# Performance work log

Hardware: AMD Instinct MI355X
Metric: run time of the kernel (lower is better)

Reference implementation:

```python
import jax, jax.numpy as jnp
import numpy as np

DIM = 1024
NUM_HEADS = 16
HEAD_D = DIM // NUM_HEADS


def setup_inputs() -> dict:
    key = jax.random.key(0)
    ks = jax.random.split(key, 9)
    s = 1.0 / np.sqrt(DIM)
    x = jax.random.normal(ks[0], (2, 2048, DIM), dtype=jnp.float32)
    Wq = jax.random.uniform(ks[1], (DIM, DIM), jnp.float32, -s, s)
    bq = jax.random.uniform(ks[2], (DIM,), jnp.float32, -s, s)
    Wk = jax.random.uniform(ks[3], (DIM, DIM), jnp.float32, -s, s)
    bk = jax.random.uniform(ks[4], (DIM,), jnp.float32, -s, s)
    Wv = jax.random.uniform(ks[5], (DIM, DIM), jnp.float32, -s, s)
    bv = jax.random.uniform(ks[6], (DIM,), jnp.float32, -s, s)
    Wo = jax.random.uniform(ks[7], (DIM, DIM), jnp.float32, -s, s)
    bo = jax.random.uniform(ks[8], (DIM,), jnp.float32, -s, s)
    return {"x": x, "Wq": Wq, "bq": bq, "Wk": Wk, "bk": bk,
            "Wv": Wv, "bv": bv, "Wo": Wo, "bo": bo}


def reference(x, Wq, bq, Wk, bk, Wv, bv, Wo, bo):
    B, T, D = x.shape
    H, Hd = NUM_HEADS, HEAD_D
    # torch Linear: x @ W.T + b
    q = (x @ Wq.T + bq).reshape(B, T, H, Hd).transpose(0, 2, 1, 3)  # [B,H,T,Hd]
    k = (x @ Wk.T + bk).reshape(B, T, H, Hd).transpose(0, 2, 1, 3)
    v = (x @ Wv.T + bv).reshape(B, T, H, Hd).transpose(0, 2, 1, 3)
    scores = jnp.einsum('bhqd,bhkd->bhqk', q, k) / jnp.sqrt(jnp.float32(Hd))
    causal = jnp.tril(jnp.ones((T, T), dtype=bool))  # [T,T]
    scores = jnp.where(causal[None, None], scores, -jnp.inf)
    probs = jax.nn.softmax(scores, axis=-1)
    ctx = jnp.einsum('bhqk,bhkd->bhqd', probs, v)
    out = ctx.transpose(0, 2, 1, 3).reshape(B, T, D)
    out = out @ Wo.T + bo
    return (out, (k, v))
```

## Files before the change

### kernel.cpp

```cpp
#include <hip/hip_runtime.h>

#define BB 2
#define TT 2048
#define DD 1024
#define HH 16
#define HD 64
#define MM (BB*TT)

typedef __bf16 bf16;
typedef __bf16 bf16x4 __attribute__((ext_vector_type(4)));
typedef __bf16 bf16x8 __attribute__((ext_vector_type(8)));
typedef float  f32x4  __attribute__((ext_vector_type(4)));

#define QSCALE 0.1803368801111244f
#define M0 16.0f

__device__ __forceinline__ void gl_lds16(const void* g, void* l) {
  __builtin_amdgcn_global_load_lds(
      (const __attribute__((address_space(1))) void*)g,
      (__attribute__((address_space(3))) void*)l, 16, 0, 0);
}
__device__ __forceinline__ f32x4 mfma16(bf16x8 a, bf16x8 b, f32x4 c) {
  return __builtin_amdgcn_mfma_f32_16x16x32_bf16(a, b, c, 0, 0, 0);
}

__global__ void cvt_all(const float* __restrict__ x,
                        const float* __restrict__ w0, const float* __restrict__ w1,
                        const float* __restrict__ w2, const float* __restrict__ w3,
                        bf16* __restrict__ xd,
                        bf16* __restrict__ d0, bf16* __restrict__ d1,
                        bf16* __restrict__ d2, bf16* __restrict__ d3) {
  int i = blockIdx.x * blockDim.x + threadIdx.x;
  const float* s;
  bf16* d;
  int off;
  if (i < (1 << 20)) { s = x; d = xd; off = i; }
  else {
    int j = (i - (1 << 20)) >> 18;
    off = (i - (1 << 20)) & ((1 << 18) - 1);
    s = (j == 0) ? w0 : (j == 1) ? w1 : (j == 2) ? w2 : w3;
    d = (j == 0) ? d0 : (j == 1) ? d1 : (j == 2) ? d2 : d3;
  }
  float4 v = ((const float4*)s)[off];
  bf16x4 o = { (bf16)v.x, (bf16)v.y, (bf16)v.z, (bf16)v.w };
  ((bf16x4*)d)[off] = o;
}

__launch_bounds__(512)
__global__ void gemm_qkv(const bf16* __restrict__ X,
                         const bf16* __restrict__ Wq, const bf16* __restrict__ Wk,
                         const bf16* __restrict__ Wv,
                         const float* __restrict__ bq, const float* __restrict__ bk,
                         const float* __restrict__ bv,
                         bf16* __restrict__ qb, bf16* __restrict__ kb,
                         bf16* __restrict__ vtb,
                         float* __restrict__ kf, float* __restrict__ vf) {
  __shared__ bf16 sA[128 * 32];
  __shared__ bf16 sB[2][128 * 32];
  const int tid  = threadIdx.x;
  const int wv   = tid >> 6;
  const int lane = tid & 63;
  const int quad = lane >> 4, l15 = lane & 15;
  const int wy   = wv >> 1, wx = wv & 1;
  const int g    = blockIdx.x >> 4;
  const int j    = blockIdx.x & 15;
  const int row  = tid >> 2;
  const int c8   = ((tid & 3) ^ ((row >> 1) & 3)) * 8;
  const int rsw  = (l15 >> 1) & 3;
  char* lA  = (char*)sA    + wv * 1024;
  char* lB0 = (char*)sB[0] + wv * 1024;
  char* lB1 = (char*)sB[1] + wv * 1024;

  if (j < 8) {
    const int m0 = g * 128;
    const int n0 = j * 128;
    const bf16* Ab  = X  + (size_t)(m0 + row) * DD + c8;
    const bf16* Bqb = Wq + (size_t)(n0 + row) * DD + c8;
    const bf16* Bkb = Wk + (size_t)(n0 + row) * DD + c8;
    f32x4 accq[2][4] = {}, acck[2][4] = {};
    for (int k0 = 0; k0 < DD; k0 += 32) {
      gl_lds16(Ab  + k0, lA);
      gl_lds16(Bqb + k0, lB0);
      gl_lds16(Bkb + k0, lB1);
      __syncthreads();
      bf16x8 af[2], bq_[4], bk_[4];
#pragma unroll
      for (int mi = 0; mi < 2; mi++)
        af[mi] = *(const bf16x8*)(sA + (wy * 32 + mi * 16 + l15) * 32
                                     + ((quad ^ rsw) * 8));
#pragma unroll
      for (int ni = 0; ni < 4; ni++) {
        bq_[ni] = *(const bf16x8*)(sB[0] + (wx * 64 + ni * 16 + l15) * 32
                                         + ((quad ^ rsw) * 8));
        bk_[ni] = *(const bf16x8*)(sB[1] + (wx * 64 + ni * 16 + l15) * 32
                                         + ((quad ^ rsw) * 8));
      }
#pragma unroll
      for (int mi = 0; mi < 2; mi++)
#pragma unroll
        for (int ni = 0; ni < 4; ni++) {
          accq[mi][ni] = mfma16(af[mi], bq_[ni], accq[mi][ni]);
          acck[mi][ni] = mfma16(af[mi], bk_[ni], acck[mi][ni]);
        }
      __syncthreads();
    }
    for (int mi = 0; mi < 2; mi++)
      for (int ni = 0; ni < 4; ni++)
        for (int r = 0; r < 4; r++) {
          int m = m0 + wy * 32 + mi * 16 + quad * 4 + r;
          int n = n0 + wx * 64 + ni * 16 + l15;
          int b = m >> 11, t = m & (TT - 1);
          int h = n >> 6,  d = n & (HD - 1);
          size_t idx = ((size_t)(b * HH + h) * TT + t) * HD + d;
          qb[idx] = (bf16)((accq[mi][ni][r] + bq[n]) * QSCALE);
          float vk = acck[mi][ni][r] + bk[n];
          kb[idx] = (bf16)vk;
          kf[idx] = vk;
        }
  } else {
    const int m0 = (j - 8) * 128;
    const int n0 = g * 128;
    const bf16* Ab = Wv + (size_t)(m0 + row) * DD + c8;
    const bf16* Bb = X  + (size_t)(n0 + row) * DD + c8;
    f32x4 acc[2][4] = {};
    for (int k0 = 0; k0 < DD; k0 += 32) {
      gl_lds16(Ab + k0, lA);
      gl_lds16(Bb + k0, lB0);
      __syncthreads();
      bf16x8 af[2], bx_[4];
#pragma unroll
      for (int mi = 0; mi < 2; mi++)
        af[mi] = *(const bf16x8*)(sA + (wy * 32 + mi * 16 + l15) * 32
                                     + ((quad ^ rsw) * 8));
#pragma unroll
      for (int ni = 0; ni < 4; ni++)
        bx_[ni] = *(const bf16x8*)(sB[0] + (wx * 64 + ni * 16 + l15) * 32
                                        + ((quad ^ rsw) * 8));
#pragma unroll
      for (int mi = 0; mi < 2; mi++)
#pragma unroll
        for (int ni = 0; ni < 4; ni++)
          acc[mi][ni] = mfma16(af[mi], bx_[ni], acc[mi][ni]);
      __syncthreads();
    }
    for (int mi = 0; mi < 2; mi++) {
      int mbase = m0 + wy * 32 + mi * 16 + quad * 4;
      float brv[4];
      for (int r = 0; r < 4; r++) brv[r] = bv[mbase + r];
      int h = mbase >> 6, dbase = mbase & (HD - 1);
      for (int ni = 0; ni < 4; ni++) {
        int tok = n0 + wx * 64 + ni * 16 + l15;
        int b = tok >> 11, t = tok & (TT - 1);
        int bh = b * HH + h;
        float4 vv;
        float* vp = &vv.x;
        for (int r = 0; r < 4; r++) {
          float v = acc[mi][ni][r] + brv[r];
          vp[r] = v;
          vtb[((size_t)bh * HD + dbase + r) * TT + t] = (bf16)v;
        }
        *(float4*)&vf[((size_t)bh * TT + t) * HD + dbase] = vv;
      }
    }
  }
}

template<int BM, int BN>
__device__ __forceinline__ void tile_core64(const bf16* __restrict__ A,
                                            const bf16* __restrict__ W,
                                            int m0, int n0,
                                            bf16* sA, bf16* sB,
                                            f32x4 (&acc)[BM/32][BN/32]) {
  const int tid  = threadIdx.x;
  const int wv   = tid >> 6;
  const int l15  = tid & 15;
  const int quad = (tid & 63) >> 4;
  const int wy   = wv >> 1, wx = wv & 1;
  const int MI_  = BM / 32, NI_ = BN / 32;
  const int srow = tid >> 3;
  const int schk = (tid & 7) ^ (srow & 7);
  const int rswz = l15 & 7;
  const bf16* Ab = A + (size_t)(m0 + srow) * DD + schk * 8;
  const bf16* Wb = W + (size_t)(n0 + srow) * DD + schk * 8;
  char* lA = (char*)sA + wv * 1024;
  char* lB = (char*)sB + wv * 1024;
  for (int k0 = 0; k0 < DD; k0 += 64) {
#pragma unroll
    for (int j = 0; j < BM / 32; j++)
      gl_lds16(Ab + (size_t)j * 32 * DD + k0, lA + j * 4096);
#pragma unroll
    for (int j = 0; j < BN / 32; j++)
      gl_lds16(Wb + (size_t)j * 32 * DD + k0, lB + j * 4096);
    __syncthreads();
#pragma unroll
    for (int h = 0; h < 2; h++) {
      bf16x8 af[MI_], bw[NI_];
#pragma unroll
      for (int mi = 0; mi < MI_; mi++)
        af[mi] = *(const bf16x8*)(sA + (wy * (BM / 2) + mi * 16 + l15) * 64
                                     + (((h * 4 + quad) ^ rswz) * 8));
#pragma unroll
      for (int ni = 0; ni < NI_; ni++)
        bw[ni] = *(const bf16x8*)(sB + (wx * (BN / 2) + ni * 16 + l15) * 64
                                     + (((h * 4 + quad) ^ rswz) * 8));
#pragma unroll
      for (int mi = 0; mi < MI_; mi++)
#pragma unroll
        for (int ni = 0; ni < NI_; ni++)
          acc[mi][ni] = mfma16(af[mi], bw[ni], acc[mi][ni]);
    }
    __syncthreads();
  }
}

__launch_bounds__(256)
__global__ void gemm_o(const bf16* __restrict__ A, const bf16* __restrict__ W,
                       const float* __restrict__ bias, float* __restrict__ out) {
  __shared__ bf16 sA[64 * 64];
  __shared__ bf16 sB[128 * 64];
  const int m0 = blockIdx.x * 64;
  const int n0 = blockIdx.y * 128;
  f32x4 acc[2][4] = {};
  tile_core64<64, 128>(A, W, m0, n0, sA, sB, acc);
  const int wv = threadIdx.x >> 6;
  const int l15 = threadIdx.x & 15, quad = (threadIdx.x & 63) >> 4;
  const int wy = wv >> 1, wx = wv & 1;
  for (int mi = 0; mi < 2; mi++)
    for (int ni = 0; ni < 4; ni++)
      for (int r = 0; r < 4; r++) {
        int m = m0 + wy * 32 + mi * 16 + quad * 4 + r;
        int n = n0 + wx * 64 + ni * 16 + l15;
        out[(size_t)m * DD + n] = acc[mi][ni][r] + bias[n];
      }
}

__launch_bounds__(256, 4)
__global__ void attn_fwd(const bf16* __restrict__ Q, const bf16* __restrict__ Kg,
                         const bf16* __restrict__ Vt, bf16* __restrict__ ctx) {
  __shared__ __align__(16) bf16 kbuf[2][4096];
  __shared__ __align__(16) bf16 vbuf[2][4096];
  __shared__ __align__(16) bf16 pbuf[4][1024];
  const int tid  = threadIdx.x;
  const int lane = tid & 63, wv = tid >> 6;
  const int quad = lane >> 4, l15 = lane & 15;
  const int bx = blockIdx.x;
  const int sl = bx >> 3;
  const int c  = 31 - (sl >> 2);
  const int bh = (bx & 7) + 8 * (sl & 3);
  const int qr = c * 64 + wv * 16;
  const int ntiles = c + 1;

  const bf16* Kbh = Kg + (size_t)bh * TT * HD;
  const bf16* Vbh = Vt + (size_t)bh * HD * TT;

  const int k0s = tid >> 3,  c0s = (tid & 7) ^ (k0s & 7);
  const int s1  = 256 + tid;
  const int k1s = s1 >> 3,   c1s = (s1 & 7) ^ (k1s & 7);

  int foff[4][2];
  for (int sub = 0; sub < 4; sub++)
    for (int h = 0; h < 2; h++)
      foff[sub][h] = (((sub * 16 + l15) * 8) + ((h * 4 + quad) ^ (l15 & 7))) * 8;

  const bf16* qp = Q + ((size_t)bh * TT + qr + l15) * HD + quad * 8;
  bf16x8 aq0 = *(const bf16x8*)qp;
  bf16x8 aq1 = *(const bf16x8*)(qp + 32);

  float lrow = 0.f;
  f32x4 acc[4] = {};
  bf16* pb = pbuf[wv];
  const int pswz = l15 & 7;

  gl_lds16(Kbh + (size_t)k0s * HD + c0s * 8, (char*)kbuf[0] + wv * 1024);
  gl_lds16(Kbh + (size_t)k1s * HD + c1s * 8, (char*)kbuf[0] + 4096 + wv * 1024);
  gl_lds16(Vbh + (size_t)k0s * TT + c0s * 8, (char*)vbuf[0] + wv * 1024);
  gl_lds16(Vbh + (size_t)k1s * TT + c1s * 8, (char*)vbuf[0] + 4096 + wv * 1024);

  for (int t = 0; t < ntiles; t++) {
    const int kt = t * 64;
    __syncthreads();
    if (t + 1 < ntiles) {
      bf16* kn = kbuf[(t + 1) & 1];
      bf16* vn = vbuf[(t + 1) & 1];
      gl_lds16(Kbh + (size_t)(kt + 64 + k0s) * HD + c0s * 8, (char*)kn + wv * 1024);
      gl_lds16(Kbh + (size_t)(kt + 64 + k1s) * HD + c1s * 8, (char*)kn + 4096 + wv * 1024);
      gl_lds16(Vbh + (size_t)k0s * TT + kt + 64 + c0s * 8, (char*)vn + wv * 1024);
      gl_lds16(Vbh + (size_t)k1s * TT + kt + 64 + c1s * 8, (char*)vn + 4096 + wv * 1024);
    }
    const bf16* kc = kbuf[t & 1];
    const bf16* vc = vbuf[t & 1];
    const bool last = (t == ntiles - 1);

    float p[4][4];
    for (int sub = 0; sub < 4; sub++) {
      if (last && kt + sub * 16 > qr + 15) {
        p[sub][0] = p[sub][1] = p[sub][2] = p[sub][3] = 0.f;
        continue;
      }
      bf16x8 ak0 = *(const bf16x8*)(kc + foff[sub][0]);
      bf16x8 ak1 = *(const bf16x8*)(kc + foff[sub][1]);
      f32x4 z = {};
      f32x4 st = mfma16(ak0, aq0, z);
      st = mfma16(ak1, aq1, st);
      if (last) {
        for (int r = 0; r < 4; r++) {
          int k_abs = kt + sub * 16 + quad * 4 + r;
          p[sub][r] = (k_abs > qr + l15) ? 0.f
                      : __builtin_amdgcn_exp2f(st[r] - M0);
        }
      } else {
        for (int r = 0; r < 4; r++)
          p[sub][r] = __builtin_amdgcn_exp2f(st[r] - M0);
      }
      lrow += (p[sub][0] + p[sub][1]) + (p[sub][2] + p[sub][3]);
    }

    for (int sub = 0; sub < 4; sub++) {
      bf16x4 pk = { (bf16)p[sub][0], (bf16)p[sub][1], (bf16)p[sub][2], (bf16)p[sub][3] };
      int cch = sub * 2 + (quad >> 1);
      *(bf16x4*)&pb[l15 * 64 + ((cch ^ pswz) * 8 + (quad & 1) * 4)] = pk;
    }
    bf16x8 ap0 = *(const bf16x8*)&pb[l15 * 64 + ((quad ^ pswz) * 8)];
    bf16x8 ap1 = *(const bf16x8*)&pb[l15 * 64 + (((4 + quad) ^ pswz) * 8)];

    for (int ni = 0; ni < 4; ni++) {
      bf16x8 v0 = *(const bf16x8*)(vc + foff[ni][0]);
      bf16x8 v1 = *(const bf16x8*)(vc + foff[ni][1]);
      acc[ni] = mfma16(ap0, v0, acc[ni]);
      acc[ni] = mfma16(ap1, v1, acc[ni]);
    }
  }

  lrow += __shfl_xor(lrow, 16, 64);
  lrow += __shfl_xor(lrow, 32, 64);
  float invl = 1.f / lrow;
  float invq[4];
  for (int r = 0; r < 4; r++)
    invq[r] = __shfl(invl, (lane & 48) | (quad * 4 + r), 64);
  int b = bh >> 4, h = bh & (HH - 1);
  for (int ni = 0; ni < 4; ni++)
    for (int r = 0; r < 4; r++) {
      int tq = qr + quad * 4 + r;
      ctx[((size_t)(b * TT + tq)) * DD + h * HD + ni * 16 + l15] = (bf16)(acc[ni][r] * invq[r]);
    }
}

extern "C" void kernel_launch(void* const* d_in, const int* in_sizes, int n_in,
                              void* d_out, int out_size, void* d_ws, size_t ws_size,
                              hipStream_t stream) {
  const float* x  = (const float*)d_in[0];
  const float* Wq = (const float*)d_in[1];
  const float* bq = (const float*)d_in[2];
  const float* Wk = (const float*)d_in[3];
  const float* bk = (const float*)d_in[4];
  const float* Wv = (const float*)d_in[5];
  const float* bv = (const float*)d_in[6];
  const float* Wo = (const float*)d_in[7];
  const float* bo = (const float*)d_in[8];
  float* out = (float*)d_out;
  float* outK = out + (size_t)MM * DD;
  float* outV = out + (size_t)2 * MM * DD;

  char* ws = (char*)d_ws;
  bf16* xb   = (bf16*)(ws);
  bf16* wqb  = (bf16*)(ws + (8  << 20));
  bf16* wkb  = (bf16*)(ws + (10 << 20));
  bf16* wvb  = (bf16*)(ws + (12 << 20));
  bf16* wob  = (bf16*)(ws + (14 << 20));
  bf16* qbuf = (bf16*)(ws + (16 << 20));
  bf16* kbuf = (bf16*)(ws + (24 << 20));
  bf16* vtb  = (bf16*)(ws + (32 << 20));
  bf16* ctxb = (bf16*)(ws + (40 << 20));

  cvt_all<<<(2 << 20) / 256, 256, 0, stream>>>(x, Wq, Wk, Wv, Wo,
                                               xb, wqb, wkb, wvb, wob);

  gemm_qkv<<<512, 512, 0, stream>>>(xb, wqb, wkb, wvb, bq, bk, bv,
                                    qbuf, kbuf, vtb, outK, outV);

  attn_fwd<<<1024, 256, 0, stream>>>(qbuf, kbuf, vtb, ctxb);

  gemm_o<<<dim3(MM / 64, DD / 128), 256, 0, stream>>>(ctxb, wob, bo, out);
}
```

Baseline: 181.7 us.

## Double-buffer LDS tiles in QKV and output-projection GEMMs

Both the fused QKV GEMM and the output-projection GEMM now keep two LDS buffers per operand. The next K-slice is prefetched with global_load_lds while MFMAs run on the current buffer, with one barrier per iteration instead of two. The aim is to hide global-load latency behind matrix math. In exchange, shared-memory use per block doubles, which can reduce how many blocks fit on each compute unit.

New measurement: 200.6 us. 10.4% more time.

```diff
diff --git a/kernel.cpp b/kernel.cpp
--- a/kernel.cpp
+++ b/kernel.cpp
@@ -55,8 +55,8 @@
                          bf16* __restrict__ qb, bf16* __restrict__ kb,
                          bf16* __restrict__ vtb,
                          float* __restrict__ kf, float* __restrict__ vf) {
-  __shared__ bf16 sA[128 * 32];
-  __shared__ bf16 sB[2][128 * 32];
+  __shared__ bf16 sA[2][128 * 32];
+  __shared__ bf16 sB[2][2][128 * 32];
   const int tid  = threadIdx.x;
   const int wv   = tid >> 6;
   const int lane = tid & 63;
@@ -65,11 +65,9 @@
   const int g    = blockIdx.x >> 4;
   const int j    = blockIdx.x & 15;
   const int row  = tid >> 2;
-  const int c8   = ((tid & 3) ^ ((row >> 1) & 3)) * 8;
+  const int c8   = ((tid & 3) ^ ((row >> 1) & 3)) * 4 * 2;
   const int rsw  = (l15 >> 1) & 3;
-  char* lA  = (char*)sA    + wv * 1024;
-  char* lB0 = (char*)sB[0] + wv * 1024;
-  char* lB1 = (char*)sB[1] + wv * 1024;
+  const int ldst = wv * 1024;
 
   if (j < 8) {
     const int m0 = g * 128;
@@ -78,22 +76,31 @@
     const bf16* Bqb = Wq + (size_t)(n0 + row) * DD + c8;
     const bf16* Bkb = Wk + (size_t)(n0 + row) * DD + c8;
     f32x4 accq[2][4] = {}, acck[2][4] = {};
+    gl_lds16(Ab,  (char*)sA[0]    + ldst);
+    gl_lds16(Bqb, (char*)sB[0][0] + ldst);
+    gl_lds16(Bkb, (char*)sB[0][1] + ldst);
+    __syncthreads();
+    int cur = 0;
     for (int k0 = 0; k0 < DD; k0 += 32) {
-      gl_lds16(Ab  + k0, lA);
-      gl_lds16(Bqb + k0, lB0);
-      gl_lds16(Bkb + k0, lB1);
-      __syncthreads();
+      if (k0 + 32 < DD) {
+        gl_lds16(Ab  + k0 + 32, (char*)sA[cur ^ 1]    + ldst);
+        gl_lds16(Bqb + k0 + 32, (char*)sB[cur ^ 1][0] + ldst);
+        gl_lds16(Bkb + k0 + 32, (char*)sB[cur ^ 1][1] + ldst);
+      }
+      const bf16* cA = sA[cur];
+      const bf16* cq = sB[cur][0];
+      const bf16* ck = sB[cur][1];
       bf16x8 af[2], bq_[4], bk_[4];
 #pragma unroll
       for (int mi = 0; mi < 2; mi++)
-        af[mi] = *(const bf16x8*)(sA + (wy * 32 + mi * 16 + l15) * 32
+        af[mi] = *(const bf16x8*)(cA + (wy * 32 + mi * 16 + l15) * 32
                                      + ((quad ^ rsw) * 8));
 #pragma unroll
       for (int ni = 0; ni < 4; ni++) {
-        bq_[ni] = *(const bf16x8*)(sB[0] + (wx * 64 + ni * 16 + l15) * 32
-                                         + ((quad ^ rsw) * 8));
-        bk_[ni] = *(const bf16x8*)(sB[1] + (wx * 64 + ni * 16 + l15) * 32
-                                         + ((quad ^ rsw) * 8));
+        bq_[ni] = *(const bf16x8*)(cq + (wx * 64 + ni * 16 + l15) * 32
+                                      + ((quad ^ rsw) * 8));
+        bk_[ni] = *(const bf16x8*)(ck + (wx * 64 + ni * 16 + l15) * 32
+                                      + ((quad ^ rsw) * 8));
       }
 #pragma unroll
       for (int mi = 0; mi < 2; mi++)
@@ -103,6 +110,7 @@
           acck[mi][ni] = mfma16(af[mi], bk_[ni], acck[mi][ni]);
         }
       __syncthreads();
+      cur ^= 1;
     }
     for (int mi = 0; mi < 2; mi++)
       for (int ni = 0; ni < 4; ni++)
@@ -123,25 +131,33 @@
     const bf16* Ab = Wv + (size_t)(m0 + row) * DD + c8;
     const bf16* Bb = X  + (size_t)(n0 + row) * DD + c8;
     f32x4 acc[2][4] = {};
+    gl_lds16(Ab, (char*)sA[0]    + ldst);
+    gl_lds16(Bb, (char*)sB[0][0] + ldst);
+    __syncthreads();
+    int cur = 0;
     for (int k0 = 0; k0 < DD; k0 += 32) {
-      gl_lds16(Ab + k0, lA);
-      gl_lds16(Bb + k0, lB0);
-      __syncthreads();
+      if (k0 + 32 < DD) {
+        gl_lds16(Ab + k0 + 32, (char*)sA[cur ^ 1]    + ldst);
+        gl_lds16(Bb + k0 + 32, (char*)sB[cur ^ 1][0] + ldst);
+      }
+      const bf16* cA = sA[cur];
+      const bf16* cB = sB[cur][0];
       bf16x8 af[2], bx_[4];
 #pragma unroll
       for (int mi = 0; mi < 2; mi++)
-        af[mi] = *(const bf16x8*)(sA + (wy * 32 + mi * 16 + l15) * 32
+        af[mi] = *(const bf16x8*)(cA + (wy * 32 + mi * 16 + l15) * 32
                                      + ((quad ^ rsw) * 8));
 #pragma unroll
       for (int ni = 0; ni < 4; ni++)
-        bx_[ni] = *(const bf16x8*)(sB[0] + (wx * 64 + ni * 16 + l15) * 32
-                                        + ((quad ^ rsw) * 8));
+        bx_[ni] = *(const bf16x8*)(cB + (wx * 64 + ni * 16 + l15) * 32
+                                     + ((quad ^ rsw) * 8));
 #pragma unroll
       for (int mi = 0; mi < 2; mi++)
 #pragma unroll
         for (int ni = 0; ni < 4; ni++)
           acc[mi][ni] = mfma16(af[mi], bx_[ni], acc[mi][ni]);
       __syncthreads();
+      cur ^= 1;
     }
     for (int mi = 0; mi < 2; mi++) {
       int mbase = m0 + wy * 32 + mi * 16 + quad * 4;
@@ -169,7 +185,7 @@
 __device__ __forceinline__ void tile_core64(const bf16* __restrict__ A,
                                             const bf16* __restrict__ W,
                                             int m0, int n0,
-                                            bf16* sA, bf16* sB,
+                                            bf16 (*sA)[BM * 64], bf16 (*sB)[BN * 64],
                                             f32x4 (&acc)[BM/32][BN/32]) {
   const int tid  = threadIdx.x;
   const int wv   = tid >> 6;
@@ -182,26 +198,36 @@
   const int rswz = l15 & 7;
   const bf16* Ab = A + (size_t)(m0 + srow) * DD + schk * 8;
   const bf16* Wb = W + (size_t)(n0 + srow) * DD + schk * 8;
-  char* lA = (char*)sA + wv * 1024;
-  char* lB = (char*)sB + wv * 1024;
+  const int ldst = wv * 1024;
+#pragma unroll
+  for (int j = 0; j < BM / 32; j++)
+    gl_lds16(Ab + (size_t)j * 32 * DD, (char*)sA[0] + ldst + j * 4096);
+#pragma unroll
+  for (int j = 0; j < BN / 32; j++)
+    gl_lds16(Wb + (size_t)j * 32 * DD, (char*)sB[0] + ldst + j * 4096);
+  __syncthreads();
+  int cur = 0;
   for (int k0 = 0; k0 < DD; k0 += 64) {
-#pragma unroll
-    for (int j = 0; j < BM / 32; j++)
-      gl_lds16(Ab + (size_t)j * 32 * DD + k0, lA + j * 4096);
-#pragma unroll
-    for (int j = 0; j < BN / 32; j++)
-      gl_lds16(Wb + (size_t)j * 32 * DD + k0, lB + j * 4096);
-    __syncthreads();
+    if (k0 + 64 < DD) {
+#pragma unroll
+      for (int j = 0; j < BM / 32; j++)
+        gl_lds16(Ab + (size_t)j * 32 * DD + k0 + 64, (char*)sA[cur ^ 1] + ldst + j * 4096);
+#pragma unroll
+      for (int j = 0; j < BN / 32; j++)
+        gl_lds16(Wb + (size_t)j * 32 * DD + k0 + 64, (char*)sB[cur ^ 1] + ldst + j * 4096);
+    }
+    const bf16* cA = sA[cur];
+    const bf16* cB = sB[cur];
 #pragma unroll
     for (int h = 0; h < 2; h++) {
       bf16x8 af[MI_], bw[NI_];
 #pragma unroll
       for (int mi = 0; mi < MI_; mi++)
-        af[mi] = *(const bf16x8*)(sA + (wy * (BM / 2) + mi * 16 + l15) * 64
+        af[mi] = *(const bf16x8*)(cA + (wy * (BM / 2) + mi * 16 + l15) * 64
                                      + (((h * 4 + quad) ^ rswz) * 8));
 #pragma unroll
       for (int ni = 0; ni < NI_; ni++)
-        bw[ni] = *(const bf16x8*)(sB + (wx * (BN / 2) + ni * 16 + l15) * 64
+        bw[ni] = *(const bf16x8*)(cB + (wx * (BN / 2) + ni * 16 + l15) * 64
                                      + (((h * 4 + quad) ^ rswz) * 8));
 #pragma unroll
       for (int mi = 0; mi < MI_; mi++)
@@ -210,14 +236,15 @@
           acc[mi][ni] = mfma16(af[mi], bw[ni], acc[mi][ni]);
     }
     __syncthreads();
+    cur ^= 1;
   }
 }
 
 __launch_bounds__(256)
 __global__ void gemm_o(const bf16* __restrict__ A, const bf16* __restrict__ W,
                        const float* __restrict__ bias, float* __restrict__ out) {
-  __shared__ bf16 sA[64 * 64];
-  __shared__ bf16 sB[128 * 64];
+  __shared__ bf16 sA[2][64 * 64];
+  __shared__ bf16 sB[2][128 * 64];
   const int m0 = blockIdx.x * 64;
   const int n0 = blockIdx.y * 128;
   f32x4 acc[2][4] = {};
```

## Split QKV GEMM into 64-row tiles with 256-thread blocks and double grid

Applied to the files above, without the earlier changes.

The fused QKV projection kernel now uses 256-thread blocks covering 64x128 output tiles instead of 512-thread blocks covering 128x128, and launches 1024 blocks instead of 512. Each thread issues two direct-to-LDS loads for the B operand to fill the 128-row tile. The aim is more, smaller workgroups so the GPU's compute units are better filled and load-balanced. The cost is that each B tile is fetched by twice as many blocks, and each thread issues more loads per k-step.

Result: slower. 204.2 us (+12.4%).

```diff
diff --git a/kernel.cpp b/kernel.cpp
--- a/kernel.cpp
+++ b/kernel.cpp
@@ -46,7 +46,7 @@
   ((bf16x4*)d)[off] = o;
 }
 
-__launch_bounds__(512)
+__launch_bounds__(256)
 __global__ void gemm_qkv(const bf16* __restrict__ X,
                          const bf16* __restrict__ Wq, const bf16* __restrict__ Wk,
                          const bf16* __restrict__ Wv,
@@ -55,33 +55,33 @@
                          bf16* __restrict__ qb, bf16* __restrict__ kb,
                          bf16* __restrict__ vtb,
                          float* __restrict__ kf, float* __restrict__ vf) {
-  __shared__ bf16 sA[128 * 32];
+  __shared__ bf16 sA[64 * 32];
   __shared__ bf16 sB[2][128 * 32];
   const int tid  = threadIdx.x;
   const int wv   = tid >> 6;
   const int lane = tid & 63;
   const int quad = lane >> 4, l15 = lane & 15;
   const int wy   = wv >> 1, wx = wv & 1;
-  const int g    = blockIdx.x >> 4;
-  const int j    = blockIdx.x & 15;
+  const int G    = blockIdx.x >> 5;
+  const int u    = blockIdx.x & 31;
   const int row  = tid >> 2;
   const int c8   = ((tid & 3) ^ ((row >> 1) & 3)) * 8;
   const int rsw  = (l15 >> 1) & 3;
-  char* lA  = (char*)sA    + wv * 1024;
-  char* lB0 = (char*)sB[0] + wv * 1024;
-  char* lB1 = (char*)sB[1] + wv * 1024;
-
-  if (j < 8) {
-    const int m0 = g * 128;
-    const int n0 = j * 128;
+  const int ldst = wv * 1024;
+
+  if (u < 16) {
+    const int m0 = (2 * G + (u >> 3)) * 64;
+    const int n0 = (u & 7) * 128;
     const bf16* Ab  = X  + (size_t)(m0 + row) * DD + c8;
     const bf16* Bqb = Wq + (size_t)(n0 + row) * DD + c8;
     const bf16* Bkb = Wk + (size_t)(n0 + row) * DD + c8;
     f32x4 accq[2][4] = {}, acck[2][4] = {};
     for (int k0 = 0; k0 < DD; k0 += 32) {
-      gl_lds16(Ab  + k0, lA);
-      gl_lds16(Bqb + k0, lB0);
-      gl_lds16(Bkb + k0, lB1);
+      gl_lds16(Ab  + k0,           (char*)sA    + ldst);
+      gl_lds16(Bqb + k0,           (char*)sB[0] + ldst);
+      gl_lds16(Bqb + 64 * DD + k0, (char*)sB[0] + 4096 + ldst);
+      gl_lds16(Bkb + k0,           (char*)sB[1] + ldst);
+      gl_lds16(Bkb + 64 * DD + k0, (char*)sB[1] + 4096 + ldst);
       __syncthreads();
       bf16x8 af[2], bq_[4], bk_[4];
 #pragma unroll
@@ -118,14 +118,15 @@
           kf[idx] = vk;
         }
   } else {
-    const int m0 = (j - 8) * 128;
-    const int n0 = g * 128;
+    const int m0 = (u - 16) * 64;
+    const int n0 = G * 128;
     const bf16* Ab = Wv + (size_t)(m0 + row) * DD + c8;
     const bf16* Bb = X  + (size_t)(n0 + row) * DD + c8;
     f32x4 acc[2][4] = {};
     for (int k0 = 0; k0 < DD; k0 += 32) {
-      gl_lds16(Ab + k0, lA);
-      gl_lds16(Bb + k0, lB0);
+      gl_lds16(Ab + k0,           (char*)sA    + ldst);
+      gl_lds16(Bb + k0,           (char*)sB[0] + ldst);
+      gl_lds16(Bb + 64 * DD + k0, (char*)sB[0] + 4096 + ldst);
       __syncthreads();
       bf16x8 af[2], bx_[4];
 #pragma unroll
@@ -375,8 +376,8 @@
   cvt_all<<<(2 << 20) / 256, 256, 0, stream>>>(x, Wq, Wk, Wv, Wo,
                                                xb, wqb, wkb, wvb, wob);
 
-  gemm_qkv<<<512, 512, 0, stream>>>(xb, wqb, wkb, wvb, bq, bk, bv,
-                                    qbuf, kbuf, vtb, outK, outV);
+  gemm_qkv<<<1024, 256, 0, stream>>>(xb, wqb, wkb, wvb, bq, bk, bv,
+                                     qbuf, kbuf, vtb, outK, outV);
 
   attn_fwd<<<1024, 256, 0, stream>>>(qbuf, kbuf, vtb, ctxb);
 
```
